# Optimization experiments

Measured on AMD Instinct MI355X. Metric: run time of the kernel, lower is better.

## Reference

```python
import jax, jax.numpy as jnp
import numpy as np

L = 80
INTERVAL = 5
NCPT = int(np.ceil(L / INTERVAL)) + 1          # 17
INTERVAL2 = 1 if INTERVAL == 1 else L - (NCPT - 2) * INTERVAL  # 5
N = (L + 1) ** 2                                # 6561
REPEATS = np.array([2 * l + 1 for l in range(L + 1)])  # static, sums to N


def setup_inputs() -> dict:
    key = jax.random.key(0)
    k1, k2 = jax.random.split(key)
    in_ch, out_ch, batch = 64, 64, 32
    x = jax.random.normal(k1, (batch, in_ch, N), dtype=jnp.float32)
    stdv = 1.0 / np.sqrt(in_ch * (L + 1))
    weight = jax.random.uniform(k2, (in_ch, out_ch, NCPT, 1),
                                dtype=jnp.float32, minval=-stdv, maxval=stdv)
    return {"x": x, "weight": weight}


def reference(x, weight):
    # interpolation coefficients (constants, match torch buffers)
    l0 = jnp.tile(jnp.arange(INTERVAL, dtype=jnp.float32) / INTERVAL,
                  (NCPT - 2, 1))                       # (ncpt-2, interval)
    l1 = (jnp.arange(INTERVAL2 + 1, dtype=jnp.float32) / INTERVAL2)[None, :]  # (1, interval2+1)

    in_ch, out_ch = weight.shape[0], weight.shape[1]
    # linear interpolation between anchor points
    w1 = ((1.0 - l0) * weight[:, :, :-2, :] + l0 * weight[:, :, 1:-1, :])
    w1 = w1.reshape(in_ch, out_ch, -1)                 # (in, out, (ncpt-2)*interval)
    w2 = ((1.0 - l1) * weight[:, :, -2:-1, :] + l1 * weight[:, :, -1:, :])
    w2 = w2.reshape(in_ch, out_ch, -1)                 # (in, out, interval2+1)
    w_l = jnp.concatenate([w1, w2], axis=2)            # (in, out, L+1)

    # expand per-degree coeff to 2l+1 orders -> (in, out, (L+1)^2)
    w = jnp.repeat(w_l, REPEATS, axis=2, total_repeat_length=N)

    # per-position channel mixing: sum over in_ch, no (b,in,out,N) intermediate
    return jnp.einsum('bin,ion->bon', x, w)
```

## Files before the change

### kernel.cpp

```cpp
#include <hip/hip_runtime.h>
#include <hip/hip_bf16.h>


#define NTOT 6561
#define NL   81
#define CH   64
#define NSLOTS 451
#define WTB_BYTES (NL * CH * CH * 2)

typedef __attribute__((ext_vector_type(8))) short bf16x8;
typedef __attribute__((ext_vector_type(4))) float f32x4;

__global__ __launch_bounds__(256) void interp_bf16(const float* __restrict__ w,
                                                   __hip_bfloat16* __restrict__ wtb) {
  int idx = blockIdx.x * 256 + threadIdx.x;
  int l = idx >> 12;
  int o = (idx >> 6) & 63;
  int i = idx & 63;
  int cp; float f;
  if (l < 75) { cp = l / 5; f = (float)(l - cp * 5) * 0.2f; }
  else        { cp = 15;    f = (float)(l - 75) * 0.2f; }
  const float* wp = w + (size_t)(i * 64 + o) * 17 + cp;
  float v = (1.0f - f) * wp[0] + f * wp[1];
  wtb[(size_t)l * 4096 + o * 64 + i] = __float2bfloat16(v);
}

__device__ __forceinline__ void load_item(const float* __restrict__ xb,
                                          float (&xr)[16], int kg) {
#pragma unroll
  for (int ks = 0; ks < 2; ++ks)
#pragma unroll
    for (int j = 0; j < 8; ++j)
      xr[ks * 8 + j] = xb[(size_t)(ks * 32 + kg * 8 + j) * NTOT];
}

__device__ __forceinline__ void compute_store(const float (&xr)[16],
                                              const bf16x8 (&afrag)[2][4],
                                              float* __restrict__ ob,
                                              bool act, int kg) {
  bf16x8 bf[2];
#pragma unroll
  for (int ks = 0; ks < 2; ++ks)
#pragma unroll
    for (int j = 0; j < 8; ++j) {
      __hip_bfloat16 h = __float2bfloat16(xr[ks * 8 + j]);
      bf[ks][j] = *reinterpret_cast<short*>(&h);
    }
  f32x4 acc[4];
#pragma unroll
  for (int t = 0; t < 4; ++t) acc[t] = (f32x4)(0.0f);
#pragma unroll
  for (int ks = 0; ks < 2; ++ks)
#pragma unroll
    for (int t = 0; t < 4; ++t)
      acc[t] = __builtin_amdgcn_mfma_f32_16x16x32_bf16(afrag[ks][t], bf[ks], acc[t], 0, 0, 0);
  if (act) {
#pragma unroll
    for (int t = 0; t < 4; ++t)
#pragma unroll
      for (int rg = 0; rg < 4; ++rg)
        ob[(size_t)(t * 16 + kg * 4 + rg) * NTOT] = acc[t][rg];
  }
}

__global__ __launch_bounds__(256) void shconv_pipe(const float* __restrict__ x,
                                                   const __hip_bfloat16* __restrict__ wtb,
                                                   float* __restrict__ out) {
  const int wv   = threadIdx.x >> 6;
  const int lane = threadIdx.x & 63;
  const int m    = lane & 15;
  const int kg   = lane >> 4;
  const int s    = (int)blockIdx.x * 4 + wv;
  if (s >= NSLOTS) return;
  const int bq   = blockIdx.y;

  int g = 0;
  while (g < 10 && 4 * (g + 1) * (g + 2) <= s) ++g;
  const int r = s - 4 * g * (g + 1);
  const int l = 8 * g + r / (g + 1);
  const int c = r - (l - 8 * g) * (g + 1);
  const int P = 2 * l + 1;

  const int p  = c * 16 + m;
  const int pl = (p < P) ? p : (P - 1);
  const bool act = (p < P);
  const size_t nbase = (size_t)l * l;

  const __hip_bfloat16* wl = wtb + (size_t)l * 4096;
  bf16x8 afrag[2][4];
#pragma unroll
  for (int ks = 0; ks < 2; ++ks)
#pragma unroll
    for (int t = 0; t < 4; ++t)
      afrag[ks][t] = *reinterpret_cast<const bf16x8*>(
          wl + (size_t)(t * 16 + m) * 64 + ks * 32 + kg * 8);

  const int b0 = bq * 4;
  const float* xp0 = x + (size_t)(b0 + 0) * CH * NTOT + nbase + pl;
  const float* xp1 = x + (size_t)(b0 + 1) * CH * NTOT + nbase + pl;
  const float* xp2 = x + (size_t)(b0 + 2) * CH * NTOT + nbase + pl;
  const float* xp3 = x + (size_t)(b0 + 3) * CH * NTOT + nbase + pl;
  float* op0 = out + (size_t)(b0 + 0) * CH * NTOT + nbase + p;
  float* op1 = out + (size_t)(b0 + 1) * CH * NTOT + nbase + p;
  float* op2 = out + (size_t)(b0 + 2) * CH * NTOT + nbase + p;
  float* op3 = out + (size_t)(b0 + 3) * CH * NTOT + nbase + p;

  float xrA[16], xrB[16];
  load_item(xp0, xrA, kg);
  load_item(xp1, xrB, kg);
  compute_store(xrA, afrag, op0, act, kg);
  load_item(xp2, xrA, kg);
  compute_store(xrB, afrag, op1, act, kg);
  load_item(xp3, xrB, kg);
  compute_store(xrA, afrag, op2, act, kg);
  compute_store(xrB, afrag, op3, act, kg);
}

__global__ __launch_bounds__(192) void shconv_fallback(const float* __restrict__ x,
                                                       const float* __restrict__ w,
                                                       float* __restrict__ out) {
  __shared__ float wl[2][64][64];
  const int l1 = blockIdx.x;
  const int l2 = 80 - l1;
  const int P1 = 2 * l1 + 1;
  const int P2 = (l1 == 40) ? 0 : 2 * l2 + 1;
  int cp1, cp2; float f1, f2;
  if (l1 < 75) { cp1 = l1 / 5; f1 = (float)(l1 - cp1 * 5) * 0.2f; }
  else         { cp1 = 15;     f1 = (float)(l1 - 75) * 0.2f; }
  if (l2 < 75) { cp2 = l2 / 5; f2 = (float)(l2 - cp2 * 5) * 0.2f; }
  else         { cp2 = 15;     f2 = (float)(l2 - 75) * 0.2f; }
  const int tid = threadIdx.x;
  for (int e = tid; e < 8192; e += 192) {
    int sel = e >> 12, rr = e & 4095, i = rr >> 6, o = rr & 63;
    int cp = sel ? cp2 : cp1;
    float f = sel ? f2 : f1;
    const float* wp = w + (size_t)(i * 64 + o) * 17 + cp;
    wl[sel][i][o] = (1.0f - f) * wp[0] + f * wp[1];
  }
  __syncthreads();
  const int Ptot = P1 + P2;
  if (tid >= Ptot) return;
  int sel, l, p;
  if (tid < P1) { sel = 0; l = l1; p = tid; }
  else          { sel = 1; l = l2; p = tid - P1; }
  const size_t nidx = (size_t)(l * l) + p;
  const int b0 = blockIdx.y, b1 = b0 + 16;
  const float* x0 = x + (size_t)b0 * CH * NTOT + nidx;
  const float* x1 = x + (size_t)b1 * CH * NTOT + nidx;
  float acc0[64], acc1[64];
#pragma unroll
  for (int o = 0; o < 64; ++o) { acc0[o] = 0.f; acc1[o] = 0.f; }
  const float* wbase = &wl[sel][0][0];
#pragma unroll 4
  for (int i = 0; i < 64; ++i) {
    float xv0 = x0[(size_t)i * NTOT];
    float xv1 = x1[(size_t)i * NTOT];
    const float* wr = wbase + i * 64;
#pragma unroll
    for (int o = 0; o < 64; o += 4) {
      float4 wv = *(const float4*)(wr + o);
      acc0[o]     = fmaf(xv0, wv.x, acc0[o]);
      acc0[o + 1] = fmaf(xv0, wv.y, acc0[o + 1]);
      acc0[o + 2] = fmaf(xv0, wv.z, acc0[o + 2]);
      acc0[o + 3] = fmaf(xv0, wv.w, acc0[o + 3]);
      acc1[o]     = fmaf(xv1, wv.x, acc1[o]);
      acc1[o + 1] = fmaf(xv1, wv.y, acc1[o + 1]);
      acc1[o + 2] = fmaf(xv1, wv.z, acc1[o + 2]);
      acc1[o + 3] = fmaf(xv1, wv.w, acc1[o + 3]);
    }
  }
  float* o0 = out + (size_t)b0 * CH * NTOT + nidx;
  float* o1 = out + (size_t)b1 * CH * NTOT + nidx;
#pragma unroll
  for (int o = 0; o < 64; ++o) {
    o0[(size_t)o * NTOT] = acc0[o];
    o1[(size_t)o * NTOT] = acc1[o];
  }
}

extern "C" void kernel_launch(void* const* d_in, const int* in_sizes, int n_in,
                              void* d_out, int out_size, void* d_ws, size_t ws_size,
                              hipStream_t stream) {
  const float* x = (const float*)d_in[0];
  const float* w = (const float*)d_in[1];
  float* out = (float*)d_out;

  if (ws_size >= (size_t)WTB_BYTES && d_ws != nullptr) {
    __hip_bfloat16* wtb = (__hip_bfloat16*)d_ws;
    hipLaunchKernelGGL(interp_bf16, dim3(1296), dim3(256), 0, stream, w, wtb);
    hipLaunchKernelGGL(shconv_pipe, dim3(113, 8), dim3(256), 0, stream, x, wtb, out);
  } else {
    hipLaunchKernelGGL(shconv_fallback, dim3(41, 16), dim3(192), 0, stream, x, w, out);
  }
}
```

Baseline: 36.16 us.

## Process two positions per lane with 8-byte loads and stores, halving wave slots

Each lane now covers two adjacent spherical-harmonic positions, loading and storing them as float2, and runs two MFMA sets that share the same weight fragments. Waves now cover 32 positions instead of 16, so the slot count and grid roughly halve and the weight-fragment loads are amortised over twice the work. The aim is wider memory transactions and less per-slot overhead. In exchange, register pressure rises, edge handling becomes more complex because of even-aligned bases and the last element, and there are fewer waves to hide latency.

```diff
diff --git a/kernel.cpp b/kernel.cpp
--- a/kernel.cpp
+++ b/kernel.cpp
@@ -5,7 +5,7 @@
 #define NTOT 6561
 #define NL   81
 #define CH   64
-#define NSLOTS 451
+#define NSLOT32 246
 #define WTB_BYTES (NL * CH * CH * 2)
 
 typedef __attribute__((ext_vector_type(8))) short bf16x8;
@@ -25,66 +25,91 @@
   wtb[(size_t)l * 4096 + o * 64 + i] = __float2bfloat16(v);
 }
 
-__device__ __forceinline__ void load_item(const float* __restrict__ xb,
-                                          float (&xr)[16], int kg) {
+__device__ __forceinline__ void load_item2(const float* __restrict__ xb,
+                                           float2 (&xr)[16], int kg) {
 #pragma unroll
   for (int ks = 0; ks < 2; ++ks)
 #pragma unroll
     for (int j = 0; j < 8; ++j)
-      xr[ks * 8 + j] = xb[(size_t)(ks * 32 + kg * 8 + j) * NTOT];
-}
-
-__device__ __forceinline__ void compute_store(const float (&xr)[16],
-                                              const bf16x8 (&afrag)[2][4],
-                                              float* __restrict__ ob,
-                                              bool act, int kg) {
-  bf16x8 bf[2];
+      __builtin_memcpy(&xr[ks * 8 + j],
+                       xb + (size_t)(ks * 32 + kg * 8 + j) * NTOT, 8);
+}
+
+__device__ __forceinline__ void compute_store2(const float2 (&xr)[16],
+                                               const bf16x8 (&afrag)[2][4],
+                                               float* __restrict__ ob,
+                                               bool v0, bool v1, bool sh, int kg) {
+  bf16x8 bfA[2], bfB[2];
 #pragma unroll
   for (int ks = 0; ks < 2; ++ks)
 #pragma unroll
     for (int j = 0; j < 8; ++j) {
-      __hip_bfloat16 h = __float2bfloat16(xr[ks * 8 + j]);
-      bf[ks][j] = *reinterpret_cast<short*>(&h);
-    }
-  f32x4 acc[4];
-#pragma unroll
-  for (int t = 0; t < 4; ++t) acc[t] = (f32x4)(0.0f);
-#pragma unroll
-  for (int ks = 0; ks < 2; ++ks)
-#pragma unroll
-    for (int t = 0; t < 4; ++t)
-      acc[t] = __builtin_amdgcn_mfma_f32_16x16x32_bf16(afrag[ks][t], bf[ks], acc[t], 0, 0, 0);
-  if (act) {
-#pragma unroll
-    for (int t = 0; t < 4; ++t)
-#pragma unroll
-      for (int rg = 0; rg < 4; ++rg)
-        ob[(size_t)(t * 16 + kg * 4 + rg) * NTOT] = acc[t][rg];
-  }
-}
-
-__global__ __launch_bounds__(256) void shconv_pipe(const float* __restrict__ x,
-                                                   const __hip_bfloat16* __restrict__ wtb,
-                                                   float* __restrict__ out) {
+      __hip_bfloat16 hA = __float2bfloat16(xr[ks * 8 + j].x);
+      __hip_bfloat16 hB = __float2bfloat16(xr[ks * 8 + j].y);
+      bfA[ks][j] = *reinterpret_cast<short*>(&hA);
+      bfB[ks][j] = *reinterpret_cast<short*>(&hB);
+    }
+  f32x4 accA[4], accB[4];
+#pragma unroll
+  for (int t = 0; t < 4; ++t) { accA[t] = (f32x4)(0.0f); accB[t] = (f32x4)(0.0f); }
+#pragma unroll
+  for (int ks = 0; ks < 2; ++ks)
+#pragma unroll
+    for (int t = 0; t < 4; ++t) {
+      accA[t] = __builtin_amdgcn_mfma_f32_16x16x32_bf16(afrag[ks][t], bfA[ks], accA[t], 0, 0, 0);
+      accB[t] = __builtin_amdgcn_mfma_f32_16x16x32_bf16(afrag[ks][t], bfB[ks], accB[t], 0, 0, 0);
+    }
+#pragma unroll
+  for (int t = 0; t < 4; ++t)
+#pragma unroll
+    for (int rg = 0; rg < 4; ++rg) {
+      float* op = ob + (size_t)(t * 16 + kg * 4 + rg) * NTOT;
+      if (v0 && v1) {
+        float2 sv; sv.x = accA[t][rg]; sv.y = accB[t][rg];
+        __builtin_memcpy(op, &sv, 8);
+      } else if (v1) {
+        op[1] = accB[t][rg];
+      } else if (v0) {
+        op[0] = sh ? accB[t][rg] : accA[t][rg];
+      }
+    }
+}
+
+__global__ __launch_bounds__(256) void shconv_pipe2(const float* __restrict__ x,
+                                                    const __hip_bfloat16* __restrict__ wtb,
+                                                    float* __restrict__ out) {
   const int wv   = threadIdx.x >> 6;
   const int lane = threadIdx.x & 63;
   const int m    = lane & 15;
   const int kg   = lane >> 4;
   const int s    = (int)blockIdx.x * 4 + wv;
-  if (s >= NSLOTS) return;
+  if (s >= NSLOT32) return;
   const int bq   = blockIdx.y;
 
-  int g = 0;
-  while (g < 10 && 4 * (g + 1) * (g + 2) <= s) ++g;
-  const int r = s - 4 * g * (g + 1);
-  const int l = 8 * g + r / (g + 1);
-  const int c = r - (l - 8 * g) * (g + 1);
-  const int P = 2 * l + 1;
-
-  const int p  = c * 16 + m;
-  const int pl = (p < P) ? p : (P - 1);
-  const bool act = (p < P);
-  const size_t nbase = (size_t)l * l;
+  int l, c;
+  if (s >= 240) { l = 80; c = s - 240; }
+  else {
+    int g = 0;
+    while (g < 4 && 8 * (g + 1) * (g + 2) <= s) ++g;
+    const int r = s - 8 * g * (g + 1);
+    const int q = r / (g + 1);
+    l = 16 * g + q;
+    c = r - q * (g + 1);
+  }
+  const int P    = 2 * l + 1;
+  const int lo   = l * l;
+  const int end  = lo + P;
+  const int base = lo & ~1;
+  const int w0   = base + c * 32;
+
+  const int gp  = w0 + 2 * m;
+  const bool v0 = (gp     >= lo) && (gp     < end);
+  const bool v1 = (gp + 1 >= lo) && (gp + 1 < end);
+  int n2 = gp; bool sh = false;
+  if (n2 > NTOT - 2) {
+    sh = (gp == NTOT - 1) && v0;
+    n2 = NTOT - 2;
+  }
 
   const __hip_bfloat16* wl = wtb + (size_t)l * 4096;
   bf16x8 afrag[2][4];
@@ -96,24 +121,24 @@
           wl + (size_t)(t * 16 + m) * 64 + ks * 32 + kg * 8);
 
   const int b0 = bq * 4;
-  const float* xp0 = x + (size_t)(b0 + 0) * CH * NTOT + nbase + pl;
-  const float* xp1 = x + (size_t)(b0 + 1) * CH * NTOT + nbase + pl;
-  const float* xp2 = x + (size_t)(b0 + 2) * CH * NTOT + nbase + pl;
-  const float* xp3 = x + (size_t)(b0 + 3) * CH * NTOT + nbase + pl;
-  float* op0 = out + (size_t)(b0 + 0) * CH * NTOT + nbase + p;
-  float* op1 = out + (size_t)(b0 + 1) * CH * NTOT + nbase + p;
-  float* op2 = out + (size_t)(b0 + 2) * CH * NTOT + nbase + p;
-  float* op3 = out + (size_t)(b0 + 3) * CH * NTOT + nbase + p;
-
-  float xrA[16], xrB[16];
-  load_item(xp0, xrA, kg);
-  load_item(xp1, xrB, kg);
-  compute_store(xrA, afrag, op0, act, kg);
-  load_item(xp2, xrA, kg);
-  compute_store(xrB, afrag, op1, act, kg);
-  load_item(xp3, xrB, kg);
-  compute_store(xrA, afrag, op2, act, kg);
-  compute_store(xrB, afrag, op3, act, kg);
+  const float* xp0 = x + (size_t)(b0 + 0) * CH * NTOT + n2;
+  const float* xp1 = x + (size_t)(b0 + 1) * CH * NTOT + n2;
+  const float* xp2 = x + (size_t)(b0 + 2) * CH * NTOT + n2;
+  const float* xp3 = x + (size_t)(b0 + 3) * CH * NTOT + n2;
+  float* op0 = out + (size_t)(b0 + 0) * CH * NTOT + gp;
+  float* op1 = out + (size_t)(b0 + 1) * CH * NTOT + gp;
+  float* op2 = out + (size_t)(b0 + 2) * CH * NTOT + gp;
+  float* op3 = out + (size_t)(b0 + 3) * CH * NTOT + gp;
+
+  float2 xrA[16], xrB[16];
+  load_item2(xp0, xrA, kg);
+  load_item2(xp1, xrB, kg);
+  compute_store2(xrA, afrag, op0, v0, v1, sh, kg);
+  load_item2(xp2, xrA, kg);
+  compute_store2(xrB, afrag, op1, v0, v1, sh, kg);
+  load_item2(xp3, xrB, kg);
+  compute_store2(xrA, afrag, op2, v0, v1, sh, kg);
+  compute_store2(xrB, afrag, op3, v0, v1, sh, kg);
 }
 
 __global__ __launch_bounds__(192) void shconv_fallback(const float* __restrict__ x,
@@ -188,7 +213,7 @@
   if (ws_size >= (size_t)WTB_BYTES && d_ws != nullptr) {
     __hip_bfloat16* wtb = (__hip_bfloat16*)d_ws;
     hipLaunchKernelGGL(interp_bf16, dim3(1296), dim3(256), 0, stream, w, wtb);
-    hipLaunchKernelGGL(shconv_pipe, dim3(113, 8), dim3(256), 0, stream, x, wtb, out);
+    hipLaunchKernelGGL(shconv_pipe2, dim3(62, 8), dim3(256), 0, stream, x, wtb, out);
   } else {
     hipLaunchKernelGGL(shconv_fallback, dim3(41, 16), dim3(192), 0, stream, x, w, out);
   }
```

Result: no change. 35.71 us (-1.2%).
